# Performance work log

Measured on AMD Instinct MI355X. Metric: run time of the kernel, lower is better.

The kernel has to match this reference:

```python
import jax, jax.numpy as jnp
import numpy as np

ROW, IN_DIM, OUT_DIM, BATCH = 64, 1024, 1024, 512


def setup_inputs() -> dict:
    key = jax.random.key(0)
    k1, k2, k3 = jax.random.split(key, 3)
    x = jax.random.normal(k1, (BATCH, ROW, IN_DIM), dtype=jnp.float32)
    # torch.nn.Linear init: U(-1/sqrt(in_dim), 1/sqrt(in_dim)) for weight and bias
    bound = 1.0 / np.sqrt(IN_DIM)
    W = jax.random.uniform(k2, (ROW, IN_DIM, OUT_DIM), minval=-bound, maxval=bound, dtype=jnp.float32)
    b = jax.random.uniform(k3, (ROW, OUT_DIM), minval=-bound, maxval=bound, dtype=jnp.float32)
    return {"x": x, "W": W, "b": b}


def reference(x, W, b):
    # per-row Linear fused into a single grouped GEMM:
    # out[b, r, o] = sum_i x[b, r, i] * W[r, i, o] + b[r, o]
    return jnp.einsum('bri,rio->bro', x, W) + b[None, :, :]
```

## Files before the change

### kernel.cpp

```cpp
#include <hip/hip_runtime.h>
#include <hip/hip_bf16.h>

#define NROW  64
#define KDIM  1024
#define NDIM  1024

typedef short bf16x8 __attribute__((ext_vector_type(8)));
typedef float f32x4  __attribute__((ext_vector_type(4)));

__device__ __forceinline__ unsigned pk2bf(float lo, float hi) {
  unsigned ulo = __builtin_bit_cast(unsigned, lo) + 0x8000u;
  unsigned uhi = __builtin_bit_cast(unsigned, hi) + 0x8000u;
  return __builtin_amdgcn_perm(uhi, ulo, 0x07060302u);
}

__global__ __launch_bounds__(256) void Group_MLP_kernel(
    const float* __restrict__ x, const float* __restrict__ W,
    const float* __restrict__ bias, float* __restrict__ out) {
  const int g   = blockIdx.x;
  const int xcd = g & 7;
  const int idx = g >> 3;
  const int r   = xcd * 8 + (idx >> 5);
  const int mb  = (idx >> 3) & 3;
  const int nb  = idx & 7;
  const int m0 = mb * 128;
  const int n0 = nb * 128;

  const int t    = threadIdx.x;
  const int l    = t & 63;
  const int wave = t >> 6;
  const int wm   = wave >> 1, wn = wave & 1;
  const int lm   = l & 15, quad = l >> 4;

  __shared__ uint4 smem4[1024];
  uint2* s2 = (uint2*)smem4;

  const int maBase = ((t >> 7) << 4) | ((t >> 1) & 15);
  const int kof    = (((t >> 5) & 3) << 3) | ((t & 1) << 2);
  const float* gA0 = x + (size_t)(m0 + maBase) * (NROW * KDIM) + r * KDIM + kof;
  const size_t ASTRIDE = (size_t)32 * (NROW * KDIM);

  const int n4 = (t >> 1) & 31;
  const int qh = (t & 1) | ((t >> 6) << 1);
  const float* gB = W + (size_t)r * (KDIM * NDIM) + (qh * 4) * NDIM + n0 + n4 * 4;
  const int baseP  = (n4 >> 2) * 64 + ((qh >> 1) & 3) * 16 + (n4 & 3) * 4;
  const int swBase = baseP ^ (n4 >> 2);
  const int hB     = qh & 1;
  const int bW     = 1024 | (swBase << 1) | hB;

  int aIdx[4], bIdx[4];
  #pragma unroll
  for (int i = 0; i < 4; ++i) aIdx[i] = (wm * 4 + i) * 64 + l;
  #pragma unroll
  for (int j = 0; j < 4; ++j) {
    int grp = wn * 4 + j;
    bIdx[j] = 512 + grp * 64 + (l ^ grp);
  }

  f32x4 acc[4][4];
  #pragma unroll
  for (int i = 0; i < 4; ++i)
    #pragma unroll
    for (int j = 0; j < 4; ++j)
      acc[i][j] = {0.f, 0.f, 0.f, 0.f};

  float4 rawA[4], rawB[4];
  uint2  cvtA[4], cvtB[4];

  #pragma unroll
  for (int i = 0; i < 4; ++i) rawA[i] = *(const float4*)(gA0 + i * ASTRIDE);
  #pragma unroll
  for (int j = 0; j < 4; ++j) rawB[j] = *(const float4*)(gB + j * NDIM);

  #pragma unroll
  for (int i = 0; i < 4; ++i) {
    cvtA[i].x = pk2bf(rawA[i].x, rawA[i].y);
    cvtA[i].y = pk2bf(rawA[i].z, rawA[i].w);
  }
  cvtB[0].x = pk2bf(rawB[0].x, rawB[1].x); cvtB[0].y = pk2bf(rawB[2].x, rawB[3].x);
  cvtB[1].x = pk2bf(rawB[0].y, rawB[1].y); cvtB[1].y = pk2bf(rawB[2].y, rawB[3].y);
  cvtB[2].x = pk2bf(rawB[0].z, rawB[1].z); cvtB[2].y = pk2bf(rawB[2].z, rawB[3].z);
  cvtB[3].x = pk2bf(rawB[0].w, rawB[1].w); cvtB[3].y = pk2bf(rawB[2].w, rawB[3].w);

  gA0 += 32;
  gB  += 32 * NDIM;
  #pragma unroll
  for (int i = 0; i < 4; ++i) rawA[i] = *(const float4*)(gA0 + i * ASTRIDE);
  #pragma unroll
  for (int j = 0; j < 4; ++j) rawB[j] = *(const float4*)(gB + j * NDIM);

  for (int ks = 0; ks < 32; ++ks) {
    __syncthreads();
    #pragma unroll
    for (int i = 0; i < 4; ++i) s2[i * 256 + t] = cvtA[i];
    #pragma unroll
    for (int c = 0; c < 4; ++c) s2[bW ^ (c << 1)] = cvtB[c];
    __syncthreads();

    bf16x8 af[4], bfr[4];
    #pragma unroll
    for (int i = 0; i < 4; ++i) af[i]  = __builtin_bit_cast(bf16x8, smem4[aIdx[i]]);
    #pragma unroll
    for (int j = 0; j < 4; ++j) bfr[j] = __builtin_bit_cast(bf16x8, smem4[bIdx[j]]);

    if (ks < 31) {
      #pragma unroll
      for (int i = 0; i < 4; ++i) {
        cvtA[i].x = pk2bf(rawA[i].x, rawA[i].y);
        cvtA[i].y = pk2bf(rawA[i].z, rawA[i].w);
      }
      cvtB[0].x = pk2bf(rawB[0].x, rawB[1].x); cvtB[0].y = pk2bf(rawB[2].x, rawB[3].x);
      cvtB[1].x = pk2bf(rawB[0].y, rawB[1].y); cvtB[1].y = pk2bf(rawB[2].y, rawB[3].y);
      cvtB[2].x = pk2bf(rawB[0].z, rawB[1].z); cvtB[2].y = pk2bf(rawB[2].z, rawB[3].z);
      cvtB[3].x = pk2bf(rawB[0].w, rawB[1].w); cvtB[3].y = pk2bf(rawB[2].w, rawB[3].w);
      if (ks < 30) {
        gA0 += 32;
        gB  += 32 * NDIM;
        #pragma unroll
        for (int i = 0; i < 4; ++i) rawA[i] = *(const float4*)(gA0 + i * ASTRIDE);
        #pragma unroll
        for (int j = 0; j < 4; ++j) rawB[j] = *(const float4*)(gB + j * NDIM);
      }
    }

    #pragma unroll
    for (int i = 0; i < 4; ++i)
      #pragma unroll
      for (int j = 0; j < 4; ++j)
        acc[i][j] = __builtin_amdgcn_mfma_f32_16x16x32_bf16(af[i], bfr[j], acc[i][j], 0, 0, 0);
  }

  const int nColBase = n0 + wn * 64 + lm;
  const int mRowBase = m0 + wm * 64 + quad * 4;
  #pragma unroll
  for (int j = 0; j < 4; ++j) {
    int n = nColBase + j * 16;
    float bv = bias[r * NDIM + n];
    #pragma unroll
    for (int i = 0; i < 4; ++i) {
      int mr = mRowBase + i * 16;
      #pragma unroll
      for (int v = 0; v < 4; ++v) {
        out[(size_t)(mr + v) * (NROW * NDIM) + r * NDIM + n] = acc[i][j][v] + bv;
      }
    }
  }
}

extern "C" void kernel_launch(void* const* d_in, const int* in_sizes, int n_in,
                              void* d_out, int out_size, void* d_ws, size_t ws_size,
                              hipStream_t stream) {
  const float* x    = (const float*)d_in[0];
  const float* W    = (const float*)d_in[1];
  const float* bias = (const float*)d_in[2];
  float* out        = (float*)d_out;
  dim3 grid(64 * 4 * 8), block(256);
  hipLaunchKernelGGL(Group_MLP_kernel, grid, block, 0, stream, x, W, bias, out);
}
```

Measured before the change: 566.4 us.

## Enlarge block tile to 256x256 with 512 threads per block

Each block now computes a 256x256 output tile with 8 waves instead of a 128x128 tile with 4 waves. The grid shrinks from 2048 to 512 blocks, and each wave computes a 128x64 sub-tile with a 8x4 MFMA accumulator array. The goal is more reuse of each fp32 global load, since this kernel streams and converts both x and W from fp32 and is likely memory-bound. The costs are roughly double the accumulator registers per thread, larger LDS use, and only 512 blocks, about two per CU, so there is less parallelism to hide latency.

```diff
diff --git a/kernel.cpp b/kernel.cpp
--- a/kernel.cpp
+++ b/kernel.cpp
@@ -14,52 +14,58 @@
   return __builtin_amdgcn_perm(uhi, ulo, 0x07060302u);
 }
 
-__global__ __launch_bounds__(256) void Group_MLP_kernel(
+__global__ __launch_bounds__(512, 2) void Group_MLP_kernel(
     const float* __restrict__ x, const float* __restrict__ W,
     const float* __restrict__ bias, float* __restrict__ out) {
   const int g   = blockIdx.x;
   const int xcd = g & 7;
   const int idx = g >> 3;
-  const int r   = xcd * 8 + (idx >> 5);
-  const int mb  = (idx >> 3) & 3;
-  const int nb  = idx & 7;
-  const int m0 = mb * 128;
-  const int n0 = nb * 128;
+  const int r   = xcd * 8 + (idx >> 3);
+  const int mb  = (idx >> 2) & 1;
+  const int nb  = idx & 3;
+  const int m0 = mb * 256;
+  const int n0 = nb * 256;
 
   const int t    = threadIdx.x;
   const int l    = t & 63;
   const int wave = t >> 6;
-  const int wm   = wave >> 1, wn = wave & 1;
+  const int wm   = wave >> 2, wn = wave & 3;
   const int lm   = l & 15, quad = l >> 4;
 
-  __shared__ uint4 smem4[1024];
+  __shared__ uint4 smem4[2048];
   uint2* s2 = (uint2*)smem4;
 
   const int maBase = ((t >> 7) << 4) | ((t >> 1) & 15);
   const int kof    = (((t >> 5) & 3) << 3) | ((t & 1) << 2);
-  const float* gA0 = x + (size_t)(m0 + maBase) * (NROW * KDIM) + r * KDIM + kof;
-  const size_t ASTRIDE = (size_t)32 * (NROW * KDIM);
+  const float* gA[4];
+  #pragma unroll
+  for (int i = 0; i < 4; ++i)
+    gA[i] = x + (size_t)(m0 + i * 64 + maBase) * (NROW * KDIM) + r * KDIM + kof;
 
-  const int n4 = (t >> 1) & 31;
-  const int qh = (t & 1) | ((t >> 6) << 1);
-  const float* gB = W + (size_t)r * (KDIM * NDIM) + (qh * 4) * NDIM + n0 + n4 * 4;
+  const int n4 = ((t >> 3) & 1) | (((t >> 5) & 1) << 1) | (((t >> 1) & 1) << 2)
+               | (((t >> 2) & 1) << 3) | (((t >> 4) & 1) << 4) | (((t >> 6) & 1) << 5);
+  const int qh = (t & 1) | (((t >> 7) & 1) << 1) | (((t >> 8) & 1) << 2);
+  const float* gB[4];
+  #pragma unroll
+  for (int j = 0; j < 4; ++j)
+    gB[j] = W + (size_t)r * (KDIM * NDIM) + (qh * 4 + j) * NDIM + n0 + n4 * 4;
   const int baseP  = (n4 >> 2) * 64 + ((qh >> 1) & 3) * 16 + (n4 & 3) * 4;
-  const int swBase = baseP ^ (n4 >> 2);
+  const int swBase = baseP ^ ((n4 >> 2) & 7);
   const int hB     = qh & 1;
-  const int bW     = 1024 | (swBase << 1) | hB;
+  const int bW     = 2048 | (swBase << 1) | hB;
 
-  int aIdx[4], bIdx[4];
+  int aIdx[8], bIdx[4];
   #pragma unroll
-  for (int i = 0; i < 4; ++i) aIdx[i] = (wm * 4 + i) * 64 + l;
+  for (int i = 0; i < 8; ++i) aIdx[i] = (wm * 8 + i) * 64 + l;
   #pragma unroll
   for (int j = 0; j < 4; ++j) {
     int grp = wn * 4 + j;
-    bIdx[j] = 512 + grp * 64 + (l ^ grp);
+    bIdx[j] = 1024 + grp * 64 + (l ^ (grp & 7));
   }
 
-  f32x4 acc[4][4];
+  f32x4 acc[8][4];
   #pragma unroll
-  for (int i = 0; i < 4; ++i)
+  for (int i = 0; i < 8; ++i)
     #pragma unroll
     for (int j = 0; j < 4; ++j)
       acc[i][j] = {0.f, 0.f, 0.f, 0.f};
@@ -68,9 +74,9 @@
   uint2  cvtA[4], cvtB[4];
 
   #pragma unroll
-  for (int i = 0; i < 4; ++i) rawA[i] = *(const float4*)(gA0 + i * ASTRIDE);
+  for (int i = 0; i < 4; ++i) rawA[i] = *(const float4*)(gA[i]);
   #pragma unroll
-  for (int j = 0; j < 4; ++j) rawB[j] = *(const float4*)(gB + j * NDIM);
+  for (int j = 0; j < 4; ++j) rawB[j] = *(const float4*)(gB[j]);
 
   #pragma unroll
   for (int i = 0; i < 4; ++i) {
@@ -82,24 +88,22 @@
   cvtB[2].x = pk2bf(rawB[0].z, rawB[1].z); cvtB[2].y = pk2bf(rawB[2].z, rawB[3].z);
   cvtB[3].x = pk2bf(rawB[0].w, rawB[1].w); cvtB[3].y = pk2bf(rawB[2].w, rawB[3].w);
 
-  gA0 += 32;
-  gB  += 32 * NDIM;
   #pragma unroll
-  for (int i = 0; i < 4; ++i) rawA[i] = *(const float4*)(gA0 + i * ASTRIDE);
+  for (int i = 0; i < 4; ++i) { gA[i] += 32; rawA[i] = *(const float4*)(gA[i]); }
   #pragma unroll
-  for (int j = 0; j < 4; ++j) rawB[j] = *(const float4*)(gB + j * NDIM);
+  for (int j = 0; j < 4; ++j) { gB[j] += 32 * NDIM; rawB[j] = *(const float4*)(gB[j]); }
 
   for (int ks = 0; ks < 32; ++ks) {
     __syncthreads();
     #pragma unroll
-    for (int i = 0; i < 4; ++i) s2[i * 256 + t] = cvtA[i];
+    for (int i = 0; i < 4; ++i) s2[i * 512 + t] = cvtA[i];
     #pragma unroll
-    for (int c = 0; c < 4; ++c) s2[bW ^ (c << 1)] = cvtB[c];
+    for (int cc = 0; cc < 4; ++cc) s2[bW ^ (cc << 1)] = cvtB[cc];
     __syncthreads();
 
-    bf16x8 af[4], bfr[4];
+    bf16x8 af[8], bfr[4];
     #pragma unroll
-    for (int i = 0; i < 4; ++i) af[i]  = __builtin_bit_cast(bf16x8, smem4[aIdx[i]]);
+    for (int i = 0; i < 8; ++i) af[i]  = __builtin_bit_cast(bf16x8, smem4[aIdx[i]]);
     #pragma unroll
     for (int j = 0; j < 4; ++j) bfr[j] = __builtin_bit_cast(bf16x8, smem4[bIdx[j]]);
 
@@ -114,30 +118,28 @@
       cvtB[2].x = pk2bf(rawB[0].z, rawB[1].z); cvtB[2].y = pk2bf(rawB[2].z, rawB[3].z);
       cvtB[3].x = pk2bf(rawB[0].w, rawB[1].w); cvtB[3].y = pk2bf(rawB[2].w, rawB[3].w);
       if (ks < 30) {
-        gA0 += 32;
-        gB  += 32 * NDIM;
         #pragma unroll
-        for (int i = 0; i < 4; ++i) rawA[i] = *(const float4*)(gA0 + i * ASTRIDE);
+        for (int i = 0; i < 4; ++i) { gA[i] += 32; rawA[i] = *(const float4*)(gA[i]); }
         #pragma unroll
-        for (int j = 0; j < 4; ++j) rawB[j] = *(const float4*)(gB + j * NDIM);
+        for (int j = 0; j < 4; ++j) { gB[j] += 32 * NDIM; rawB[j] = *(const float4*)(gB[j]); }
       }
     }
 
     #pragma unroll
-    for (int i = 0; i < 4; ++i)
+    for (int j = 0; j < 4; ++j)
       #pragma unroll
-      for (int j = 0; j < 4; ++j)
+      for (int i = 0; i < 8; ++i)
         acc[i][j] = __builtin_amdgcn_mfma_f32_16x16x32_bf16(af[i], bfr[j], acc[i][j], 0, 0, 0);
   }
 
   const int nColBase = n0 + wn * 64 + lm;
-  const int mRowBase = m0 + wm * 64 + quad * 4;
+  const int mRowBase = m0 + wm * 128 + quad * 4;
   #pragma unroll
   for (int j = 0; j < 4; ++j) {
     int n = nColBase + j * 16;
     float bv = bias[r * NDIM + n];
     #pragma unroll
-    for (int i = 0; i < 4; ++i) {
+    for (int i = 0; i < 8; ++i) {
       int mr = mRowBase + i * 16;
       #pragma unroll
       for (int v = 0; v < 4; ++v) {
@@ -154,6 +156,6 @@
   const float* W    = (const float*)d_in[1];
   const float* bias = (const float*)d_in[2];
   float* out        = (float*)d_out;
-  dim3 grid(64 * 4 * 8), block(256);
+  dim3 grid(512), block(512);
   hipLaunchKernelGGL(Group_MLP_kernel, grid, block, 0, stream, x, W, bias, out);
 }
```

Result: faster. 513.1 us (-9.4%).
